# Kernel optimization log

Hardware: AMD Instinct MI355X
Metric: run time of the kernel (lower is better)

Reference implementation:

```python
import jax, jax.numpy as jnp
import numpy as np

N_NODES = 100000
N_EDGES = 1600000
N_FEAT = 100
HIDDEN = 64
N_CLASSES = 47


def setup_inputs() -> dict:
    key = jax.random.key(0)
    k1, k2, k3, k4 = jax.random.split(key, 4)
    x = jax.random.normal(k1, (N_NODES, N_FEAT), dtype=jnp.float32)
    edge_index = jax.random.randint(k2, (2, N_EDGES), 0, N_NODES, dtype=jnp.int64)
    # Glorot-style init for GCNConv weights; zero bias (PyG default)
    W0 = jax.random.normal(k3, (N_FEAT, HIDDEN), dtype=jnp.float32) * (1.0 / np.sqrt(N_FEAT))
    b0 = jnp.zeros((HIDDEN,), dtype=jnp.float32)
    W1 = jax.random.normal(k4, (HIDDEN, N_CLASSES), dtype=jnp.float32) * (1.0 / np.sqrt(HIDDEN))
    b1 = jnp.zeros((N_CLASSES,), dtype=jnp.float32)
    return {"x": x, "edge_index": edge_index, "W0": W0, "b0": b0, "W1": W1, "b1": b1}


def _gcn_norm(edge_index, n_nodes):
    # PyG gcn_norm with add_self_loops=True, edge_weight=1
    loop = jnp.arange(n_nodes, dtype=edge_index.dtype)
    row = jnp.concatenate([edge_index[0], loop])  # source nodes
    col = jnp.concatenate([edge_index[1], loop])  # destination nodes
    ones = jnp.ones(row.shape[0], dtype=jnp.float32)
    deg = jax.ops.segment_sum(ones, col, num_segments=n_nodes)
    dinv = jnp.where(deg > 0, jax.lax.rsqrt(deg), 0.0)
    norm = dinv[row] * dinv[col]  # [E + N]
    return row, col, norm


def _gcn_conv(x, W, b, row, col, norm, n_nodes):
    # GCNConv: transform, then gather-scale-scatter aggregate, then bias
    xw = x @ W                                   # [N, out]
    msg = norm[:, None] * xw[row]                # [E+N, out]
    out = jax.ops.segment_sum(msg, col, num_segments=n_nodes)
    return out + b


def reference(x, edge_index, W0, b0, W1, b1):
    n_nodes = x.shape[0]
    row, col, norm = _gcn_norm(edge_index, n_nodes)  # same graph -> same norm per layer (cached)
    h = _gcn_conv(x, W0, b0, row, col, norm, n_nodes)
    h = jax.nn.relu(h)  # dropout is identity in eval mode
    out = _gcn_conv(h, W1, b1, row, col, norm, n_nodes)
    return out
```

## Files before the change

### kernel.cpp

```cpp
#include <hip/hip_runtime.h>
#include <hip/hip_fp16.h>

#define N_NODES   100000
#define N_EDGES   1600000
#define N_FEAT    100
#define HIDDEN    64
#define N_CLASSES 47
#define ZPAD      48
#define NBIN      ((N_NODES + 255) / 256)
#define SBLK      256
#define CHUNK     (N_EDGES / SBLK)
#define NHIST     (NBIN * SBLK)
#define WT0_ELEMS (HIDDEN * 128)
#define WT1_ELEMS (ZPAD * 64)

typedef _Float16 f16x8 __attribute__((ext_vector_type(8)));
typedef float f32x4 __attribute__((ext_vector_type(4)));


__global__ __launch_bounds__(256) void k_gscan1(const int* __restrict__ in,
                                                int* __restrict__ out,
                                                int* __restrict__ sums, int n) {
    __shared__ int tmp[256];
    int i = blockIdx.x * 256 + threadIdx.x;
    int v = (i < n) ? in[i] : 0;
    tmp[threadIdx.x] = v;
    __syncthreads();
    for (int off = 1; off < 256; off <<= 1) {
        int t = (threadIdx.x >= off) ? tmp[threadIdx.x - off] : 0;
        __syncthreads();
        tmp[threadIdx.x] += t;
        __syncthreads();
    }
    if (i < n) out[i] = tmp[threadIdx.x] - v;
    if (threadIdx.x == 255) sums[blockIdx.x] = tmp[255];
}

__global__ __launch_bounds__(512) void k_gscan2(int* __restrict__ sums, int nb) {
    __shared__ int tmp[512];
    int i = threadIdx.x;
    int v = (i < nb) ? sums[i] : 0;
    tmp[i] = v;
    __syncthreads();
    for (int off = 1; off < 512; off <<= 1) {
        int t = (i >= off) ? tmp[i - off] : 0;
        __syncthreads();
        tmp[i] += t;
        __syncthreads();
    }
    if (i < nb) sums[i] = tmp[i] - v;
}


__global__ __launch_bounds__(256) void k_hist(const int* __restrict__ ecol,
                                              int* __restrict__ gh) {
    __shared__ int lh[NBIN];
    int b = blockIdx.x, t = threadIdx.x;
    for (int i = t; i < NBIN; i += 256) lh[i] = 0;
    __syncthreads();
    int e0 = b * CHUNK;
    for (int i = t; i < CHUNK; i += 256)
        atomicAdd(&lh[ecol[e0 + i] >> 8], 1);
    __syncthreads();
    for (int i = t; i < NBIN; i += 256) gh[i * SBLK + b] = lh[i];
}

__global__ __launch_bounds__(256) void k_radix_scatter(
    const int* __restrict__ erow, const int* __restrict__ ecol,
    const int* __restrict__ gpos, const int* __restrict__ hsums,
    int* __restrict__ pairs) {
    __shared__ int lc[NBIN];
    int b = blockIdx.x, t = threadIdx.x;
    for (int i = t; i < NBIN; i += 256) lc[i] = gpos[i * SBLK + b] + hsums[i];
    __syncthreads();
    int e0 = b * CHUNK;
    for (int i = t; i < CHUNK; i += 256) {
        int e = e0 + i;
        int r = erow[e], c = ecol[e];
        int pos = atomicAdd(&lc[c >> 8], 1);
        pairs[pos] = r | ((c & 255) << 17);
    }
}

__global__ __launch_bounds__(256) void k_binfinish(
    const int* __restrict__ gpos, const int* __restrict__ hsums,
    const int* __restrict__ pairs,
    int* __restrict__ rp, float* __restrict__ dinv, int* __restrict__ eidx) {
    __shared__ int cnt[256];
    __shared__ int tmp[256];
    int b = blockIdx.x, t = threadIdx.x;
    int n0 = b << 8;
    int beg = gpos[b * SBLK] + hsums[b];
    int end = (b + 1 < NBIN) ? gpos[(b + 1) * SBLK] + hsums[b + 1] : N_EDGES;

    cnt[t] = 0;
    __syncthreads();
    for (int i = beg + t; i < end; i += 256)
        atomicAdd(&cnt[(pairs[i] >> 17) & 255], 1);
    __syncthreads();
    int v = cnt[t];
    tmp[t] = v;
    __syncthreads();
    for (int off = 1; off < 256; off <<= 1) {
        int u = (t >= off) ? tmp[t - off] : 0;
        __syncthreads();
        tmp[t] += u;
        __syncthreads();
    }
    int rpv = beg + tmp[t] - v;
    int n = n0 + t;
    if (n < N_NODES) {
        rp[n] = rpv;
        dinv[n] = rsqrtf(1.0f + (float)v);
    }
    if (b == NBIN - 1 && t == 0) rp[N_NODES] = N_EDGES;
    cnt[t] = rpv;
    __syncthreads();
    for (int i = beg + t; i < end; i += 256) {
        int p = pairs[i];
        int pos = atomicAdd(&cnt[(p >> 17) & 255], 1);
        eidx[pos] = p & 0x1FFFF;
    }
}

__global__ __launch_bounds__(256) void k_wprep(const float* __restrict__ W0,
                                               const float* __restrict__ W1,
                                               __half* __restrict__ wt0,
                                               __half* __restrict__ wt1) {
    int i = blockIdx.x * 256 + threadIdx.x;
    if (i < WT0_ELEMS) {
        int n = i >> 7, k = i & 127;
        wt0[i] = __float2half((k < N_FEAT) ? W0[k * HIDDEN + n] : 0.0f);
    } else if (i < WT0_ELEMS + WT1_ELEMS) {
        int j = i - WT0_ELEMS;
        int n = j >> 6, k = j & 63;
        wt1[j] = __float2half((n < N_CLASSES) ? W1[k * N_CLASSES + n] : 0.0f);
    }
}

__global__ __launch_bounds__(256) void k_gemm1(
    const float* __restrict__ x, const __half* __restrict__ wt0,
    const float* __restrict__ dinv, __half* __restrict__ yh) {
    int w = threadIdx.x >> 6, l = threadIdx.x & 63;
    int g = l >> 4, c16 = l & 15;
    int row = blockIdx.x * 64 + w * 16 + c16;
    int rl = (row < N_NODES) ? row : (N_NODES - 1);
    const float* xr = x + (size_t)rl * N_FEAT;

    f16x8 a[4];
    #pragma unroll
    for (int s = 0; s < 4; ++s) {
        int k0 = 32 * s + 8 * g;
        float4 f0 = (k0 + 3 < N_FEAT) ? *(const float4*)(xr + k0)
                                      : make_float4(0.f, 0.f, 0.f, 0.f);
        float4 f1 = (k0 + 7 < N_FEAT) ? *(const float4*)(xr + k0 + 4)
                                      : make_float4(0.f, 0.f, 0.f, 0.f);
        a[s][0] = (_Float16)f0.x; a[s][1] = (_Float16)f0.y;
        a[s][2] = (_Float16)f0.z; a[s][3] = (_Float16)f0.w;
        a[s][4] = (_Float16)f1.x; a[s][5] = (_Float16)f1.y;
        a[s][6] = (_Float16)f1.z; a[s][7] = (_Float16)f1.w;
    }
    f32x4 acc0 = {0,0,0,0}, acc1 = {0,0,0,0}, acc2 = {0,0,0,0}, acc3 = {0,0,0,0};
    #pragma unroll
    for (int s = 0; s < 4; ++s) {
        int ko = 32 * s + 8 * g;
        f16x8 b0 = *(const f16x8*)(wt0 + (0 * 16 + c16) * 128 + ko);
        f16x8 b1 = *(const f16x8*)(wt0 + (1 * 16 + c16) * 128 + ko);
        f16x8 b2 = *(const f16x8*)(wt0 + (2 * 16 + c16) * 128 + ko);
        f16x8 b3 = *(const f16x8*)(wt0 + (3 * 16 + c16) * 128 + ko);
        acc0 = __builtin_amdgcn_mfma_f32_16x16x32_f16(a[s], b0, acc0, 0, 0, 0);
        acc1 = __builtin_amdgcn_mfma_f32_16x16x32_f16(a[s], b1, acc1, 0, 0, 0);
        acc2 = __builtin_amdgcn_mfma_f32_16x16x32_f16(a[s], b2, acc2, 0, 0, 0);
        acc3 = __builtin_amdgcn_mfma_f32_16x16x32_f16(a[s], b3, acc3, 0, 0, 0);
    }
    int orow = blockIdx.x * 64 + w * 16 + 4 * g;
    #pragma unroll
    for (int r = 0; r < 4; ++r) {
        if (orow + r < N_NODES) {
            float di = dinv[orow + r];
            size_t base = (size_t)(orow + r) * HIDDEN + c16;
            yh[base +  0] = __float2half(di * acc0[r]);
            yh[base + 16] = __float2half(di * acc1[r]);
            yh[base + 32] = __float2half(di * acc2[r]);
            yh[base + 48] = __float2half(di * acc3[r]);
        }
    }
}

__global__ __launch_bounds__(256) void k_agg0(
    const int* __restrict__ rp, const int* __restrict__ eidx,
    const float* __restrict__ dinv, const __half* __restrict__ yh,
    const float* __restrict__ b0, __half* __restrict__ hr) {
    int t = blockIdx.x * 256 + threadIdx.x;
    int n = t >> 5;
    int hl = threadIdx.x & 31;
    if (n >= N_NODES) return;
    int beg = rp[n], end = rp[n + 1];
    int deg = end - beg;
    int se = (beg + hl < end) ? eidx[beg + hl] : 0;
    const __half2* yh2 = (const __half2*)yh;
    float2 f = __half22float2(yh2[(size_t)n * 32 + hl]);
    float ax = f.x, ay = f.y;
    int m = deg < 32 ? deg : 32;
    int base = threadIdx.x & 32;

    #pragma unroll
    for (int jb = 0; jb < 4; ++jb) {
        int J = jb * 8;
        if (m > J) {
            int s0 = __shfl(se, base + J + 0), s1 = __shfl(se, base + J + 1);
            int s2 = __shfl(se, base + J + 2), s3 = __shfl(se, base + J + 3);
            int s4 = __shfl(se, base + J + 4), s5 = __shfl(se, base + J + 5);
            int s6 = __shfl(se, base + J + 6), s7 = __shfl(se, base + J + 7);
            float2 f0 = __half22float2(yh2[(size_t)s0 * 32 + hl]);
            float2 f1 = __half22float2(yh2[(size_t)s1 * 32 + hl]);
            float2 f2 = __half22float2(yh2[(size_t)s2 * 32 + hl]);
            float2 f3 = __half22float2(yh2[(size_t)s3 * 32 + hl]);
            float2 f4 = __half22float2(yh2[(size_t)s4 * 32 + hl]);
            float2 f5 = __half22float2(yh2[(size_t)s5 * 32 + hl]);
            float2 f6 = __half22float2(yh2[(size_t)s6 * 32 + hl]);
            float2 f7 = __half22float2(yh2[(size_t)s7 * 32 + hl]);
            ax += ((m > J + 0 ? f0.x : 0.f) + (m > J + 1 ? f1.x : 0.f)) +
                  ((m > J + 2 ? f2.x : 0.f) + (m > J + 3 ? f3.x : 0.f)) +
                  ((m > J + 4 ? f4.x : 0.f) + (m > J + 5 ? f5.x : 0.f)) +
                  ((m > J + 6 ? f6.x : 0.f) + (m > J + 7 ? f7.x : 0.f));
            ay += ((m > J + 0 ? f0.y : 0.f) + (m > J + 1 ? f1.y : 0.f)) +
                  ((m > J + 2 ? f2.y : 0.f) + (m > J + 3 ? f3.y : 0.f)) +
                  ((m > J + 4 ? f4.y : 0.f) + (m > J + 5 ? f5.y : 0.f)) +
                  ((m > J + 6 ? f6.y : 0.f) + (m > J + 7 ? f7.y : 0.f));
        }
    }
    if (deg > 32) {
        for (int e = beg + 32; e < end; ++e) {
            int s = eidx[e];
            float2 fv = __half22float2(yh2[(size_t)s * 32 + hl]);
            ax += fv.x; ay += fv.y;
        }
    }
    float di = dinv[n];
    float o0 = fmaxf(di * ax + b0[2 * hl], 0.0f);
    float o1 = fmaxf(di * ay + b0[2 * hl + 1], 0.0f);
    ((__half2*)hr)[(size_t)n * 32 + hl] = __floats2half2_rn(o0, o1);
}

__global__ __launch_bounds__(256) void k_gemm2(
    const __half* __restrict__ hr, const __half* __restrict__ wt1,
    const float* __restrict__ dinv, __half* __restrict__ zh) {
    int w = threadIdx.x >> 6, l = threadIdx.x & 63;
    int g = l >> 4, c16 = l & 15;
    int row = blockIdx.x * 64 + w * 16 + c16;
    int rl = (row < N_NODES) ? row : (N_NODES - 1);

    f16x8 a0 = *(const f16x8*)(hr + (size_t)rl * 64 +  0 + 8 * g);
    f16x8 a1 = *(const f16x8*)(hr + (size_t)rl * 64 + 32 + 8 * g);
    f32x4 acc0 = {0,0,0,0}, acc1 = {0,0,0,0}, acc2 = {0,0,0,0};
    #pragma unroll
    for (int s = 0; s < 2; ++s) {
        int ko = 32 * s + 8 * g;
        f16x8 b0 = *(const f16x8*)(wt1 + (0 * 16 + c16) * 64 + ko);
        f16x8 b1 = *(const f16x8*)(wt1 + (1 * 16 + c16) * 64 + ko);
        f16x8 b2 = *(const f16x8*)(wt1 + (2 * 16 + c16) * 64 + ko);
        f16x8 av = s ? a1 : a0;
        acc0 = __builtin_amdgcn_mfma_f32_16x16x32_f16(av, b0, acc0, 0, 0, 0);
        acc1 = __builtin_amdgcn_mfma_f32_16x16x32_f16(av, b1, acc1, 0, 0, 0);
        acc2 = __builtin_amdgcn_mfma_f32_16x16x32_f16(av, b2, acc2, 0, 0, 0);
    }
    int orow = blockIdx.x * 64 + w * 16 + 4 * g;
    #pragma unroll
    for (int r = 0; r < 4; ++r) {
        if (orow + r < N_NODES) {
            float di = dinv[orow + r];
            size_t base = (size_t)(orow + r) * ZPAD + c16;
            zh[base +  0] = __float2half(di * acc0[r]);
            zh[base + 16] = __float2half(di * acc1[r]);
            zh[base + 32] = __float2half(di * acc2[r]);
        }
    }
}

__global__ __launch_bounds__(256) void k_agg1(
    const int* __restrict__ rp, const int* __restrict__ eidx,
    const float* __restrict__ dinv, const __half* __restrict__ zh,
    const float* __restrict__ b1, float* __restrict__ out) {
    int t = blockIdx.x * 256 + threadIdx.x;
    int n = t >> 5;
    int hl = threadIdx.x & 31;
    if (n >= N_NODES) return;
    int beg = rp[n], end = rp[n + 1];
    int deg = end - beg;
    int se = (beg + hl < end) ? eidx[beg + hl] : 0;
    const __half2* zh2 = (const __half2*)zh;
    float ax = 0.0f, ay = 0.0f;
    if (hl < 24) {
        float2 f = __half22float2(zh2[(size_t)n * 24 + hl]);
        ax = f.x; ay = f.y;
    }
    int m = deg < 32 ? deg : 32;
    int base = threadIdx.x & 32;

    #pragma unroll
    for (int jb = 0; jb < 4; ++jb) {
        int J = jb * 8;
        if (m > J) {
            int s0 = __shfl(se, base + J + 0), s1 = __shfl(se, base + J + 1);
            int s2 = __shfl(se, base + J + 2), s3 = __shfl(se, base + J + 3);
            int s4 = __shfl(se, base + J + 4), s5 = __shfl(se, base + J + 5);
            int s6 = __shfl(se, base + J + 6), s7 = __shfl(se, base + J + 7);
            if (hl < 24) {
                float2 f0 = __half22float2(zh2[(size_t)s0 * 24 + hl]);
                float2 f1 = __half22float2(zh2[(size_t)s1 * 24 + hl]);
                float2 f2 = __half22float2(zh2[(size_t)s2 * 24 + hl]);
                float2 f3 = __half22float2(zh2[(size_t)s3 * 24 + hl]);
                float2 f4 = __half22float2(zh2[(size_t)s4 * 24 + hl]);
                float2 f5 = __half22float2(zh2[(size_t)s5 * 24 + hl]);
                float2 f6 = __half22float2(zh2[(size_t)s6 * 24 + hl]);
                float2 f7 = __half22float2(zh2[(size_t)s7 * 24 + hl]);
                ax += ((m > J + 0 ? f0.x : 0.f) + (m > J + 1 ? f1.x : 0.f)) +
                      ((m > J + 2 ? f2.x : 0.f) + (m > J + 3 ? f3.x : 0.f)) +
                      ((m > J + 4 ? f4.x : 0.f) + (m > J + 5 ? f5.x : 0.f)) +
                      ((m > J + 6 ? f6.x : 0.f) + (m > J + 7 ? f7.x : 0.f));
                ay += ((m > J + 0 ? f0.y : 0.f) + (m > J + 1 ? f1.y : 0.f)) +
                      ((m > J + 2 ? f2.y : 0.f) + (m > J + 3 ? f3.y : 0.f)) +
                      ((m > J + 4 ? f4.y : 0.f) + (m > J + 5 ? f5.y : 0.f)) +
                      ((m > J + 6 ? f6.y : 0.f) + (m > J + 7 ? f7.y : 0.f));
            }
        }
    }
    if (deg > 32) {
        for (int e = beg + 32; e < end; ++e) {
            int s = eidx[e];
            if (hl < 24) {
                float2 fv = __half22float2(zh2[(size_t)s * 24 + hl]);
                ax += fv.x; ay += fv.y;
            }
        }
    }
    if (hl < 24) {
        float di = dinv[n];
        out[(size_t)n * N_CLASSES + 2 * hl] = di * ax + b1[2 * hl];
        if (hl < 23)
            out[(size_t)n * N_CLASSES + 2 * hl + 1] = di * ay + b1[2 * hl + 1];
    }
}

extern "C" void kernel_launch(void* const* d_in, const int* in_sizes, int n_in,
                              void* d_out, int out_size, void* d_ws, size_t ws_size,
                              hipStream_t stream) {
    const float* x  = (const float*)d_in[0];
    const int*   ei = (const int*)d_in[1];
    const float* W0 = (const float*)d_in[2];
    const float* b0 = (const float*)d_in[3];
    const float* W1 = (const float*)d_in[4];
    const float* b1 = (const float*)d_in[5];
    float* out = (float*)d_out;

    char* ws = (char*)d_ws;
    float*  dinv  = (float*)(ws);
    int*    rp    = (int*)(ws + 412 * 1024);
    int*    hsums = (int*)(ws + 824 * 1024);
    int*    gh    = (int*)(ws + 828 * 1024);
    int*    gpos  = (int*)(ws + 1232 * 1024);
    __half* wt0   = (__half*)(ws + 1640 * 1024);
    __half* wt1   = (__half*)(ws + 1660 * 1024);
    int*    eidx  = (int*)(ws + 1668 * 1024);
    __half* yh    = (__half*)(ws + 9ull * 1024 * 1024);
    __half* hr    = (__half*)(ws + 22ull * 1024 * 1024);
    int*    pairs = (int*)hr;
    __half* zh    = yh;

    const int* erow = ei;
    const int* ecol = ei + N_EDGES;

    k_hist  <<<SBLK, 256, 0, stream>>>(ecol, gh);
    k_gscan1<<<NBIN, 256, 0, stream>>>(gh, gpos, hsums, NHIST);
    k_gscan2<<<1, 512, 0, stream>>>(hsums, NBIN);
    k_radix_scatter<<<SBLK, 256, 0, stream>>>(erow, ecol, gpos, hsums, pairs);
    k_binfinish<<<NBIN, 256, 0, stream>>>(gpos, hsums, pairs, rp, dinv, eidx);

    k_wprep<<<(WT0_ELEMS + WT1_ELEMS + 255) / 256, 256, 0, stream>>>(W0, W1, wt0, wt1);

    k_gemm1<<<(N_NODES + 63) / 64, 256, 0, stream>>>(x, wt0, dinv, yh);
    k_agg0 <<<(N_NODES * 32 + 255) / 256, 256, 0, stream>>>(rp, eidx, dinv, yh, b0, hr);

    k_gemm2<<<(N_NODES + 63) / 64, 256, 0, stream>>>(hr, wt1, dinv, zh);
    k_agg1 <<<(N_NODES * 32 + 255) / 256, 256, 0, stream>>>(rp, eidx, dinv, zh, b1, out);
}
```

Measured before the change: 146.0 us.

## Fuse second-layer GEMM into first aggregation kernel via shared-memory tile

The first aggregation kernel now writes its ReLU'd hidden rows for 8 nodes into a shared-memory tile (zero-padded to 16 rows), and one wavefront runs the 64x47 MFMA projection on it, writing the dinv-scaled layer-2 input directly. This removes the separate GEMM launch and the round trip of the hidden activations through global memory. Both aggregation kernels also issue 16 neighbour gathers at once instead of 8, to raise memory-level parallelism. In exchange, each block adds a barrier and runs a tiny MFMA using only one wave, with most MFMA rows being padding. The early exit for out-of-range nodes is dropped, which relies on N_NODES being a multiple of 8.

```diff
diff --git a/kernel.cpp b/kernel.cpp
--- a/kernel.cpp
+++ b/kernel.cpp
@@ -190,45 +190,108 @@
 __global__ __launch_bounds__(256) void k_agg0(
     const int* __restrict__ rp, const int* __restrict__ eidx,
     const float* __restrict__ dinv, const __half* __restrict__ yh,
-    const float* __restrict__ b0, __half* __restrict__ hr) {
+    const float* __restrict__ b0, const __half* __restrict__ wt1,
+    __half* __restrict__ zh) {
+    __shared__ __half hs[16][64];
     int t = blockIdx.x * 256 + threadIdx.x;
     int n = t >> 5;
     int hl = threadIdx.x & 31;
-    if (n >= N_NODES) return;
+    int nl = threadIdx.x >> 5;
+
+    ((__half2*)hs)[256 + threadIdx.x] = __floats2half2_rn(0.f, 0.f);
+
     int beg = rp[n], end = rp[n + 1];
     int deg = end - beg;
     int se = (beg + hl < end) ? eidx[beg + hl] : 0;
     const __half2* yh2 = (const __half2*)yh;
-    float2 f = __half22float2(yh2[(size_t)n * 32 + hl]);
-    float ax = f.x, ay = f.y;
+    float2 fs = __half22float2(yh2[(size_t)n * 32 + hl]);
+    float ax = fs.x, ay = fs.y;
     int m = deg < 32 ? deg : 32;
     int base = threadIdx.x & 32;
 
-    #pragma unroll
-    for (int jb = 0; jb < 4; ++jb) {
-        int J = jb * 8;
-        if (m > J) {
-            int s0 = __shfl(se, base + J + 0), s1 = __shfl(se, base + J + 1);
-            int s2 = __shfl(se, base + J + 2), s3 = __shfl(se, base + J + 3);
-            int s4 = __shfl(se, base + J + 4), s5 = __shfl(se, base + J + 5);
-            int s6 = __shfl(se, base + J + 6), s7 = __shfl(se, base + J + 7);
-            float2 f0 = __half22float2(yh2[(size_t)s0 * 32 + hl]);
-            float2 f1 = __half22float2(yh2[(size_t)s1 * 32 + hl]);
-            float2 f2 = __half22float2(yh2[(size_t)s2 * 32 + hl]);
-            float2 f3 = __half22float2(yh2[(size_t)s3 * 32 + hl]);
-            float2 f4 = __half22float2(yh2[(size_t)s4 * 32 + hl]);
-            float2 f5 = __half22float2(yh2[(size_t)s5 * 32 + hl]);
-            float2 f6 = __half22float2(yh2[(size_t)s6 * 32 + hl]);
-            float2 f7 = __half22float2(yh2[(size_t)s7 * 32 + hl]);
-            ax += ((m > J + 0 ? f0.x : 0.f) + (m > J + 1 ? f1.x : 0.f)) +
-                  ((m > J + 2 ? f2.x : 0.f) + (m > J + 3 ? f3.x : 0.f)) +
-                  ((m > J + 4 ? f4.x : 0.f) + (m > J + 5 ? f5.x : 0.f)) +
-                  ((m > J + 6 ? f6.x : 0.f) + (m > J + 7 ? f7.x : 0.f));
-            ay += ((m > J + 0 ? f0.y : 0.f) + (m > J + 1 ? f1.y : 0.f)) +
-                  ((m > J + 2 ? f2.y : 0.f) + (m > J + 3 ? f3.y : 0.f)) +
-                  ((m > J + 4 ? f4.y : 0.f) + (m > J + 5 ? f5.y : 0.f)) +
-                  ((m > J + 6 ? f6.y : 0.f) + (m > J + 7 ? f7.y : 0.f));
-        }
+    {
+        int s0 = __shfl(se, base + 0),  s1 = __shfl(se, base + 1);
+        int s2 = __shfl(se, base + 2),  s3 = __shfl(se, base + 3);
+        int s4 = __shfl(se, base + 4),  s5 = __shfl(se, base + 5);
+        int s6 = __shfl(se, base + 6),  s7 = __shfl(se, base + 7);
+        int s8 = __shfl(se, base + 8),  s9 = __shfl(se, base + 9);
+        int sa = __shfl(se, base + 10), sb = __shfl(se, base + 11);
+        int sc = __shfl(se, base + 12), sd = __shfl(se, base + 13);
+        int sec = __shfl(se, base + 14), sf = __shfl(se, base + 15);
+        float2 f0 = __half22float2(yh2[(size_t)s0 * 32 + hl]);
+        float2 f1 = __half22float2(yh2[(size_t)s1 * 32 + hl]);
+        float2 f2 = __half22float2(yh2[(size_t)s2 * 32 + hl]);
+        float2 f3 = __half22float2(yh2[(size_t)s3 * 32 + hl]);
+        float2 f4 = __half22float2(yh2[(size_t)s4 * 32 + hl]);
+        float2 f5 = __half22float2(yh2[(size_t)s5 * 32 + hl]);
+        float2 f6 = __half22float2(yh2[(size_t)s6 * 32 + hl]);
+        float2 f7 = __half22float2(yh2[(size_t)s7 * 32 + hl]);
+        float2 f8 = __half22float2(yh2[(size_t)s8 * 32 + hl]);
+        float2 f9 = __half22float2(yh2[(size_t)s9 * 32 + hl]);
+        float2 fa = __half22float2(yh2[(size_t)sa * 32 + hl]);
+        float2 fb = __half22float2(yh2[(size_t)sb * 32 + hl]);
+        float2 fc = __half22float2(yh2[(size_t)sc * 32 + hl]);
+        float2 fd = __half22float2(yh2[(size_t)sd * 32 + hl]);
+        float2 fe = __half22float2(yh2[(size_t)sec * 32 + hl]);
+        float2 ff = __half22float2(yh2[(size_t)sf * 32 + hl]);
+        ax += ((m > 0  ? f0.x : 0.f) + (m > 1  ? f1.x : 0.f)) +
+              ((m > 2  ? f2.x : 0.f) + (m > 3  ? f3.x : 0.f)) +
+              ((m > 4  ? f4.x : 0.f) + (m > 5  ? f5.x : 0.f)) +
+              ((m > 6  ? f6.x : 0.f) + (m > 7  ? f7.x : 0.f)) +
+              ((m > 8  ? f8.x : 0.f) + (m > 9  ? f9.x : 0.f)) +
+              ((m > 10 ? fa.x : 0.f) + (m > 11 ? fb.x : 0.f)) +
+              ((m > 12 ? fc.x : 0.f) + (m > 13 ? fd.x : 0.f)) +
+              ((m > 14 ? fe.x : 0.f) + (m > 15 ? ff.x : 0.f));
+        ay += ((m > 0  ? f0.y : 0.f) + (m > 1  ? f1.y : 0.f)) +
+              ((m > 2  ? f2.y : 0.f) + (m > 3  ? f3.y : 0.f)) +
+              ((m > 4  ? f4.y : 0.f) + (m > 5  ? f5.y : 0.f)) +
+              ((m > 6  ? f6.y : 0.f) + (m > 7  ? f7.y : 0.f)) +
+              ((m > 8  ? f8.y : 0.f) + (m > 9  ? f9.y : 0.f)) +
+              ((m > 10 ? fa.y : 0.f) + (m > 11 ? fb.y : 0.f)) +
+              ((m > 12 ? fc.y : 0.f) + (m > 13 ? fd.y : 0.f)) +
+              ((m > 14 ? fe.y : 0.f) + (m > 15 ? ff.y : 0.f));
+    }
+    if (m > 16) {
+        int s0 = __shfl(se, base + 16), s1 = __shfl(se, base + 17);
+        int s2 = __shfl(se, base + 18), s3 = __shfl(se, base + 19);
+        int s4 = __shfl(se, base + 20), s5 = __shfl(se, base + 21);
+        int s6 = __shfl(se, base + 22), s7 = __shfl(se, base + 23);
+        int s8 = __shfl(se, base + 24), s9 = __shfl(se, base + 25);
+        int sa = __shfl(se, base + 26), sb = __shfl(se, base + 27);
+        int sc = __shfl(se, base + 28), sd = __shfl(se, base + 29);
+        int sec = __shfl(se, base + 30), sf = __shfl(se, base + 31);
+        float2 f0 = __half22float2(yh2[(size_t)s0 * 32 + hl]);
+        float2 f1 = __half22float2(yh2[(size_t)s1 * 32 + hl]);
+        float2 f2 = __half22float2(yh2[(size_t)s2 * 32 + hl]);
+        float2 f3 = __half22float2(yh2[(size_t)s3 * 32 + hl]);
+        float2 f4 = __half22float2(yh2[(size_t)s4 * 32 + hl]);
+        float2 f5 = __half22float2(yh2[(size_t)s5 * 32 + hl]);
+        float2 f6 = __half22float2(yh2[(size_t)s6 * 32 + hl]);
+        float2 f7 = __half22float2(yh2[(size_t)s7 * 32 + hl]);
+        float2 f8 = __half22float2(yh2[(size_t)s8 * 32 + hl]);
+        float2 f9 = __half22float2(yh2[(size_t)s9 * 32 + hl]);
+        float2 fa = __half22float2(yh2[(size_t)sa * 32 + hl]);
+        float2 fb = __half22float2(yh2[(size_t)sb * 32 + hl]);
+        float2 fc = __half22float2(yh2[(size_t)sc * 32 + hl]);
+        float2 fd = __half22float2(yh2[(size_t)sd * 32 + hl]);
+        float2 fe = __half22float2(yh2[(size_t)sec * 32 + hl]);
+        float2 ff = __half22float2(yh2[(size_t)sf * 32 + hl]);
+        ax += ((m > 16 ? f0.x : 0.f) + (m > 17 ? f1.x : 0.f)) +
+              ((m > 18 ? f2.x : 0.f) + (m > 19 ? f3.x : 0.f)) +
+              ((m > 20 ? f4.x : 0.f) + (m > 21 ? f5.x : 0.f)) +
+              ((m > 22 ? f6.x : 0.f) + (m > 23 ? f7.x : 0.f)) +
+              ((m > 24 ? f8.x : 0.f) + (m > 25 ? f9.x : 0.f)) +
+              ((m > 26 ? fa.x : 0.f) + (m > 27 ? fb.x : 0.f)) +
+              ((m > 28 ? fc.x : 0.f) + (m > 29 ? fd.x : 0.f)) +
+              ((m > 30 ? fe.x : 0.f) + (m > 31 ? ff.x : 0.f));
+        ay += ((m > 16 ? f0.y : 0.f) + (m > 17 ? f1.y : 0.f)) +
+              ((m > 18 ? f2.y : 0.f) + (m > 19 ? f3.y : 0.f)) +
+              ((m > 20 ? f4.y : 0.f) + (m > 21 ? f5.y : 0.f)) +
+              ((m > 22 ? f6.y : 0.f) + (m > 23 ? f7.y : 0.f)) +
+              ((m > 24 ? f8.y : 0.f) + (m > 25 ? f9.y : 0.f)) +
+              ((m > 26 ? fa.y : 0.f) + (m > 27 ? fb.y : 0.f)) +
+              ((m > 28 ? fc.y : 0.f) + (m > 29 ? fd.y : 0.f)) +
+              ((m > 30 ? fe.y : 0.f) + (m > 31 ? ff.y : 0.f));
     }
     if (deg > 32) {
         for (int e = beg + 32; e < end; ++e) {
@@ -238,42 +301,39 @@
         }
     }
     float di = dinv[n];
-    float o0 = fmaxf(di * ax + b0[2 * hl], 0.0f);
-    float o1 = fmaxf(di * ay + b0[2 * hl + 1], 0.0f);
-    ((__half2*)hr)[(size_t)n * 32 + hl] = __floats2half2_rn(o0, o1);
-}
-
-__global__ __launch_bounds__(256) void k_gemm2(
-    const __half* __restrict__ hr, const __half* __restrict__ wt1,
-    const float* __restrict__ dinv, __half* __restrict__ zh) {
-    int w = threadIdx.x >> 6, l = threadIdx.x & 63;
-    int g = l >> 4, c16 = l & 15;
-    int row = blockIdx.x * 64 + w * 16 + c16;
-    int rl = (row < N_NODES) ? row : (N_NODES - 1);
-
-    f16x8 a0 = *(const f16x8*)(hr + (size_t)rl * 64 +  0 + 8 * g);
-    f16x8 a1 = *(const f16x8*)(hr + (size_t)rl * 64 + 32 + 8 * g);
-    f32x4 acc0 = {0,0,0,0}, acc1 = {0,0,0,0}, acc2 = {0,0,0,0};
-    #pragma unroll
-    for (int s = 0; s < 2; ++s) {
-        int ko = 32 * s + 8 * g;
-        f16x8 b0 = *(const f16x8*)(wt1 + (0 * 16 + c16) * 64 + ko);
-        f16x8 b1 = *(const f16x8*)(wt1 + (1 * 16 + c16) * 64 + ko);
-        f16x8 b2 = *(const f16x8*)(wt1 + (2 * 16 + c16) * 64 + ko);
-        f16x8 av = s ? a1 : a0;
-        acc0 = __builtin_amdgcn_mfma_f32_16x16x32_f16(av, b0, acc0, 0, 0, 0);
-        acc1 = __builtin_amdgcn_mfma_f32_16x16x32_f16(av, b1, acc1, 0, 0, 0);
-        acc2 = __builtin_amdgcn_mfma_f32_16x16x32_f16(av, b2, acc2, 0, 0, 0);
-    }
-    int orow = blockIdx.x * 64 + w * 16 + 4 * g;
-    #pragma unroll
-    for (int r = 0; r < 4; ++r) {
-        if (orow + r < N_NODES) {
-            float di = dinv[orow + r];
-            size_t base = (size_t)(orow + r) * ZPAD + c16;
-            zh[base +  0] = __float2half(di * acc0[r]);
-            zh[base + 16] = __float2half(di * acc1[r]);
-            zh[base + 32] = __float2half(di * acc2[r]);
+    float2 b2 = ((const float2*)b0)[hl];
+    float o0 = fmaxf(di * ax + b2.x, 0.0f);
+    float o1 = fmaxf(di * ay + b2.y, 0.0f);
+    ((__half2*)hs)[nl * 32 + hl] = __floats2half2_rn(o0, o1);
+    __syncthreads();
+
+    if (threadIdx.x < 64) {
+        int l = threadIdx.x;
+        int g = l >> 4, c16 = l & 15;
+        f16x8 a0 = *(const f16x8*)(&hs[c16][8 * g]);
+        f16x8 a1 = *(const f16x8*)(&hs[c16][32 + 8 * g]);
+        f32x4 acc0 = {0,0,0,0}, acc1 = {0,0,0,0}, acc2 = {0,0,0,0};
+        #pragma unroll
+        for (int s = 0; s < 2; ++s) {
+            int ko = 32 * s + 8 * g;
+            f16x8 b0f = *(const f16x8*)(wt1 + (0 * 16 + c16) * 64 + ko);
+            f16x8 b1f = *(const f16x8*)(wt1 + (1 * 16 + c16) * 64 + ko);
+            f16x8 b2f = *(const f16x8*)(wt1 + (2 * 16 + c16) * 64 + ko);
+            f16x8 av = s ? a1 : a0;
+            acc0 = __builtin_amdgcn_mfma_f32_16x16x32_f16(av, b0f, acc0, 0, 0, 0);
+            acc1 = __builtin_amdgcn_mfma_f32_16x16x32_f16(av, b1f, acc1, 0, 0, 0);
+            acc2 = __builtin_amdgcn_mfma_f32_16x16x32_f16(av, b2f, acc2, 0, 0, 0);
+        }
+        if (g < 2) {
+            int nrow = blockIdx.x * 8 + 4 * g;
+            #pragma unroll
+            for (int r = 0; r < 4; ++r) {
+                float dr = dinv[nrow + r];
+                size_t bz = (size_t)(nrow + r) * ZPAD + c16;
+                zh[bz +  0] = __float2half(dr * acc0[r]);
+                zh[bz + 16] = __float2half(dr * acc1[r]);
+                zh[bz + 32] = __float2half(dr * acc2[r]);
+            }
         }
     }
 }
@@ -298,32 +358,92 @@
     int m = deg < 32 ? deg : 32;
     int base = threadIdx.x & 32;
 
-    #pragma unroll
-    for (int jb = 0; jb < 4; ++jb) {
-        int J = jb * 8;
-        if (m > J) {
-            int s0 = __shfl(se, base + J + 0), s1 = __shfl(se, base + J + 1);
-            int s2 = __shfl(se, base + J + 2), s3 = __shfl(se, base + J + 3);
-            int s4 = __shfl(se, base + J + 4), s5 = __shfl(se, base + J + 5);
-            int s6 = __shfl(se, base + J + 6), s7 = __shfl(se, base + J + 7);
-            if (hl < 24) {
-                float2 f0 = __half22float2(zh2[(size_t)s0 * 24 + hl]);
-                float2 f1 = __half22float2(zh2[(size_t)s1 * 24 + hl]);
-                float2 f2 = __half22float2(zh2[(size_t)s2 * 24 + hl]);
-                float2 f3 = __half22float2(zh2[(size_t)s3 * 24 + hl]);
-                float2 f4 = __half22float2(zh2[(size_t)s4 * 24 + hl]);
-                float2 f5 = __half22float2(zh2[(size_t)s5 * 24 + hl]);
-                float2 f6 = __half22float2(zh2[(size_t)s6 * 24 + hl]);
-                float2 f7 = __half22float2(zh2[(size_t)s7 * 24 + hl]);
-                ax += ((m > J + 0 ? f0.x : 0.f) + (m > J + 1 ? f1.x : 0.f)) +
-                      ((m > J + 2 ? f2.x : 0.f) + (m > J + 3 ? f3.x : 0.f)) +
-                      ((m > J + 4 ? f4.x : 0.f) + (m > J + 5 ? f5.x : 0.f)) +
-                      ((m > J + 6 ? f6.x : 0.f) + (m > J + 7 ? f7.x : 0.f));
-                ay += ((m > J + 0 ? f0.y : 0.f) + (m > J + 1 ? f1.y : 0.f)) +
-                      ((m > J + 2 ? f2.y : 0.f) + (m > J + 3 ? f3.y : 0.f)) +
-                      ((m > J + 4 ? f4.y : 0.f) + (m > J + 5 ? f5.y : 0.f)) +
-                      ((m > J + 6 ? f6.y : 0.f) + (m > J + 7 ? f7.y : 0.f));
-            }
+    {
+        int s0 = __shfl(se, base + 0),  s1 = __shfl(se, base + 1);
+        int s2 = __shfl(se, base + 2),  s3 = __shfl(se, base + 3);
+        int s4 = __shfl(se, base + 4),  s5 = __shfl(se, base + 5);
+        int s6 = __shfl(se, base + 6),  s7 = __shfl(se, base + 7);
+        int s8 = __shfl(se, base + 8),  s9 = __shfl(se, base + 9);
+        int sa = __shfl(se, base + 10), sb = __shfl(se, base + 11);
+        int sc = __shfl(se, base + 12), sd = __shfl(se, base + 13);
+        int sec = __shfl(se, base + 14), sf = __shfl(se, base + 15);
+        if (hl < 24) {
+            float2 f0 = __half22float2(zh2[(size_t)s0 * 24 + hl]);
+            float2 f1 = __half22float2(zh2[(size_t)s1 * 24 + hl]);
+            float2 f2 = __half22float2(zh2[(size_t)s2 * 24 + hl]);
+            float2 f3 = __half22float2(zh2[(size_t)s3 * 24 + hl]);
+            float2 f4 = __half22float2(zh2[(size_t)s4 * 24 + hl]);
+            float2 f5 = __half22float2(zh2[(size_t)s5 * 24 + hl]);
+            float2 f6 = __half22float2(zh2[(size_t)s6 * 24 + hl]);
+            float2 f7 = __half22float2(zh2[(size_t)s7 * 24 + hl]);
+            float2 f8 = __half22float2(zh2[(size_t)s8 * 24 + hl]);
+            float2 f9 = __half22float2(zh2[(size_t)s9 * 24 + hl]);
+            float2 fa = __half22float2(zh2[(size_t)sa * 24 + hl]);
+            float2 fb = __half22float2(zh2[(size_t)sb * 24 + hl]);
+            float2 fc = __half22float2(zh2[(size_t)sc * 24 + hl]);
+            float2 fd = __half22float2(zh2[(size_t)sd * 24 + hl]);
+            float2 fe = __half22float2(zh2[(size_t)sec * 24 + hl]);
+            float2 ff = __half22float2(zh2[(size_t)sf * 24 + hl]);
+            ax += ((m > 0  ? f0.x : 0.f) + (m > 1  ? f1.x : 0.f)) +
+                  ((m > 2  ? f2.x : 0.f) + (m > 3  ? f3.x : 0.f)) +
+                  ((m > 4  ? f4.x : 0.f) + (m > 5  ? f5.x : 0.f)) +
+                  ((m > 6  ? f6.x : 0.f) + (m > 7  ? f7.x : 0.f)) +
+                  ((m > 8  ? f8.x : 0.f) + (m > 9  ? f9.x : 0.f)) +
+                  ((m > 10 ? fa.x : 0.f) + (m > 11 ? fb.x : 0.f)) +
+                  ((m > 12 ? fc.x : 0.f) + (m > 13 ? fd.x : 0.f)) +
+                  ((m > 14 ? fe.x : 0.f) + (m > 15 ? ff.x : 0.f));
+            ay += ((m > 0  ? f0.y : 0.f) + (m > 1  ? f1.y : 0.f)) +
+                  ((m > 2  ? f2.y : 0.f) + (m > 3  ? f3.y : 0.f)) +
+                  ((m > 4  ? f4.y : 0.f) + (m > 5  ? f5.y : 0.f)) +
+                  ((m > 6  ? f6.y : 0.f) + (m > 7  ? f7.y : 0.f)) +
+                  ((m > 8  ? f8.y : 0.f) + (m > 9  ? f9.y : 0.f)) +
+                  ((m > 10 ? fa.y : 0.f) + (m > 11 ? fb.y : 0.f)) +
+                  ((m > 12 ? fc.y : 0.f) + (m > 13 ? fd.y : 0.f)) +
+                  ((m > 14 ? fe.y : 0.f) + (m > 15 ? ff.y : 0.f));
+        }
+    }
+    if (m > 16) {
+        int s0 = __shfl(se, base + 16), s1 = __shfl(se, base + 17);
+        int s2 = __shfl(se, base + 18), s3 = __shfl(se, base + 19);
+        int s4 = __shfl(se, base + 20), s5 = __shfl(se, base + 21);
+        int s6 = __shfl(se, base + 22), s7 = __shfl(se, base + 23);
+        int s8 = __shfl(se, base + 24), s9 = __shfl(se, base + 25);
+        int sa = __shfl(se, base + 26), sb = __shfl(se, base + 27);
+        int sc = __shfl(se, base + 28), sd = __shfl(se, base + 29);
+        int sec = __shfl(se, base + 30), sf = __shfl(se, base + 31);
+        if (hl < 24) {
+            float2 f0 = __half22float2(zh2[(size_t)s0 * 24 + hl]);
+            float2 f1 = __half22float2(zh2[(size_t)s1 * 24 + hl]);
+            float2 f2 = __half22float2(zh2[(size_t)s2 * 24 + hl]);
+            float2 f3 = __half22float2(zh2[(size_t)s3 * 24 + hl]);
+            float2 f4 = __half22float2(zh2[(size_t)s4 * 24 + hl]);
+            float2 f5 = __half22float2(zh2[(size_t)s5 * 24 + hl]);
+            float2 f6 = __half22float2(zh2[(size_t)s6 * 24 + hl]);
+            float2 f7 = __half22float2(zh2[(size_t)s7 * 24 + hl]);
+            float2 f8 = __half22float2(zh2[(size_t)s8 * 24 + hl]);
+            float2 f9 = __half22float2(zh2[(size_t)s9 * 24 + hl]);
+            float2 fa = __half22float2(zh2[(size_t)sa * 24 + hl]);
+            float2 fb = __half22float2(zh2[(size_t)sb * 24 + hl]);
+            float2 fc = __half22float2(zh2[(size_t)sc * 24 + hl]);
+            float2 fd = __half22float2(zh2[(size_t)sd * 24 + hl]);
+            float2 fe = __half22float2(zh2[(size_t)sec * 24 + hl]);
+            float2 ff = __half22float2(zh2[(size_t)sf * 24 + hl]);
+            ax += ((m > 16 ? f0.x : 0.f) + (m > 17 ? f1.x : 0.f)) +
+                  ((m > 18 ? f2.x : 0.f) + (m > 19 ? f3.x : 0.f)) +
+                  ((m > 20 ? f4.x : 0.f) + (m > 21 ? f5.x : 0.f)) +
+                  ((m > 22 ? f6.x : 0.f) + (m > 23 ? f7.x : 0.f)) +
+                  ((m > 24 ? f8.x : 0.f) + (m > 25 ? f9.x : 0.f)) +
+                  ((m > 26 ? fa.x : 0.f) + (m > 27 ? fb.x : 0.f)) +
+                  ((m > 28 ? fc.x : 0.f) + (m > 29 ? fd.x : 0.f)) +
+                  ((m > 30 ? fe.x : 0.f) + (m > 31 ? ff.x : 0.f));
+            ay += ((m > 16 ? f0.y : 0.f) + (m > 17 ? f1.y : 0.f)) +
+                  ((m > 18 ? f2.y : 0.f) + (m > 19 ? f3.y : 0.f)) +
+                  ((m > 20 ? f4.y : 0.f) + (m > 21 ? f5.y : 0.f)) +
+                  ((m > 22 ? f6.y : 0.f) + (m > 23 ? f7.y : 0.f)) +
+                  ((m > 24 ? f8.y : 0.f) + (m > 25 ? f9.y : 0.f)) +
+                  ((m > 26 ? fa.y : 0.f) + (m > 27 ? fb.y : 0.f)) +
+                  ((m > 28 ? fc.y : 0.f) + (m > 29 ? fd.y : 0.f)) +
+                  ((m > 30 ? fe.y : 0.f) + (m > 31 ? ff.y : 0.f));
         }
     }
     if (deg > 32) {
@@ -364,9 +484,8 @@
     __half* wt1   = (__half*)(ws + 1660 * 1024);
     int*    eidx  = (int*)(ws + 1668 * 1024);
     __half* yh    = (__half*)(ws + 9ull * 1024 * 1024);
-    __half* hr    = (__half*)(ws + 22ull * 1024 * 1024);
-    int*    pairs = (int*)hr;
-    __half* zh    = yh;
+    __half* zh    = (__half*)(ws + 22ull * 1024 * 1024);
+    int*    pairs = (int*)zh;
 
     const int* erow = ei;
     const int* ecol = ei + N_EDGES;
@@ -380,8 +499,7 @@
     k_wprep<<<(WT0_ELEMS + WT1_ELEMS + 255) / 256, 256, 0, stream>>>(W0, W1, wt0, wt1);
 
     k_gemm1<<<(N_NODES + 63) / 64, 256, 0, stream>>>(x, wt0, dinv, yh);
-    k_agg0 <<<(N_NODES * 32 + 255) / 256, 256, 0, stream>>>(rp, eidx, dinv, yh, b0, hr);
-
-    k_gemm2<<<(N_NODES + 63) / 64, 256, 0, stream>>>(hr, wt1, dinv, zh);
-    k_agg1 <<<(N_NODES * 32 + 255) / 256, 256, 0, stream>>>(rp, eidx, dinv, zh, b1, out);
-}
+    k_agg0 <<<(N_NODES * 32) / 256, 256, 0, stream>>>(rp, eidx, dinv, yh, b0, wt1, zh);
+
+    k_agg1 <<<(N_NODES * 32) / 256, 256, 0, stream>>>(rp, eidx, dinv, zh, b1, out);
+}
```

After: 137.1 us. 6.1% less time.
